# Performance work log

Measured on AMD Instinct MI355X. Metric: run time of the kernel, lower is better.

Reference implementation:

```python
import jax, jax.numpy as jnp
import numpy as np

N, D_IN, D_H, D_OUT, M = 256, 768, 768, 512, 100000


def setup_inputs() -> dict:
    key = jax.random.key(0)
    ks = jax.random.split(key, 8)
    img_feats = jax.random.normal(ks[0], (N, D_IN), dtype=jnp.float32)
    w1 = jax.random.normal(ks[1], (D_H, D_IN), dtype=jnp.float32) * (1.0 / np.sqrt(D_IN))
    b1 = jax.random.normal(ks[2], (D_H,), dtype=jnp.float32) * 0.01
    w2 = jax.random.normal(ks[3], (D_OUT, D_H), dtype=jnp.float32) * (1.0 / np.sqrt(D_H))
    b2 = jax.random.normal(ks[4], (D_OUT,), dtype=jnp.float32) * 0.01
    logit_scale = jnp.asarray(np.log(1.0 / 0.07), dtype=jnp.float32)
    loc = jax.random.normal(ks[5], (M, D_OUT), dtype=jnp.float32)
    loc_feats = loc / jnp.linalg.norm(loc, axis=1, keepdims=True)  # pre-normalized gallery
    gps_gallery = jax.random.uniform(ks[6], (M, 2), dtype=jnp.float32, minval=-90.0, maxval=90.0)
    return {
        "img_feats": img_feats, "w1": w1, "b1": b1, "w2": w2, "b2": b2,
        "logit_scale": logit_scale, "loc_feats": loc_feats,
        "gps_gallery": gps_gallery, "top_k": 5,
    }


def reference(img_feats, w1, b1, w2, b2, logit_scale, loc_feats, gps_gallery, top_k):
    # Tsfm MLP head: Linear -> ReLU -> Linear
    h = jax.nn.relu(img_feats @ w1.T + b1)            # [N, D_H]
    img = h @ w2.T + b2                               # [N, D_OUT]
    # F.normalize(dim=1)
    img_n = img / jnp.linalg.norm(img, axis=1, keepdims=True)
    # forward_cached: scaled cosine-similarity logits against 100K gallery
    logits = jnp.exp(logit_scale) * (img_n @ loc_feats.T)  # [N, M]
    # predict: softmax over full gallery row, then top-k retrieval
    probs = jax.nn.softmax(logits, axis=-1)
    top_vals, top_idx = jax.lax.top_k(probs, top_k)   # [N, k]
    top_pred_gps = gps_gallery[top_idx[0]]            # [k, 2] (first image, as in original)
    top_pred_prob = top_vals[0]                       # [k]
    return (logits, top_pred_gps, top_pred_prob)
```

## Files before the change

kernel.cpp:

```cpp
#include <hip/hip_runtime.h>
#include <math.h>

#define N_IMG 256
#define DIN   768
#define DH    768
#define DOUT  512
#define M_GAL 100000
#define CAP   2048
#define MT    1568

typedef __bf16 bf16_t;
typedef __bf16 bf16x8 __attribute__((ext_vector_type(8)));
typedef float  f32x4  __attribute__((ext_vector_type(4)));
typedef float  f32x16 __attribute__((ext_vector_type(16)));

#define OFF_H      0
#define OFF_IMG    (N_IMG*DH)
#define OFF_IMGN   (OFF_IMG  + N_IMG*DOUT)
#define OFF_IMGT   (OFF_IMGN + N_IMG*DOUT)
#define OFF_STATS  (OFF_IMGT + N_IMG*DOUT/2)
#define OFF_CIDX   (OFF_STATS + 4)
#define OFF_CVAL   (OFF_CIDX + CAP)

#define OUT_GPS  ((size_t)N_IMG * (size_t)M_GAL)
#define OUT_PROB (OUT_GPS + 10)

__device__ inline unsigned fkey(float x) {
  unsigned u = __float_as_uint(x);
  return (u & 0x80000000u) ? ~u : (u | 0x80000000u);
}
__device__ inline float fkey_inv(unsigned k) {
  unsigned u = (k & 0x80000000u) ? (k ^ 0x80000000u) : ~k;
  return __uint_as_float(u);
}

template<int KDIM, int NCOLS, bool RELU>
__global__ __launch_bounds__(256) void mlp_gemm(const float* __restrict__ A,
    const float* __restrict__ B, const float* __restrict__ bias,
    float* __restrict__ C, unsigned* stats_init) {
  if (stats_init && blockIdx.x == 0 && blockIdx.y == 0 && threadIdx.x == 0) {
    stats_init[0] = 0u; stats_init[1] = 0u; stats_init[2] = 0u;
  }
  __shared__ float As[32][34];
  __shared__ float Bs[32][34];
  const int t  = threadIdx.x;
  const int rowbase = blockIdx.y * 32;
  const int colbase = blockIdx.x * 32;
  const int sm = t >> 3;
  const int kc = (t & 7) << 2;
  const int ty = t >> 4, tx = t & 15;
  float a00 = 0.f, a01 = 0.f, a10 = 0.f, a11 = 0.f;
  for (int kt = 0; kt < KDIM; kt += 32) {
    float4 av = *(const float4*)(A + (size_t)(rowbase + sm) * KDIM + kt + kc);
    float4 bv = *(const float4*)(B + (size_t)(colbase + sm) * KDIM + kt + kc);
    __syncthreads();
    As[kc+0][sm] = av.x; As[kc+1][sm] = av.y; As[kc+2][sm] = av.z; As[kc+3][sm] = av.w;
    Bs[kc+0][sm] = bv.x; Bs[kc+1][sm] = bv.y; Bs[kc+2][sm] = bv.z; Bs[kc+3][sm] = bv.w;
    __syncthreads();
#pragma unroll
    for (int j = 0; j < 32; ++j) {
      float2 a = *(const float2*)(&As[j][2*ty]);
      float2 b = *(const float2*)(&Bs[j][2*tx]);
      a00 = fmaf(a.x, b.x, a00); a01 = fmaf(a.x, b.y, a01);
      a10 = fmaf(a.y, b.x, a10); a11 = fmaf(a.y, b.y, a11);
    }
  }
  const int r0 = rowbase + 2*ty;
  const int c0 = colbase + 2*tx;
  const float bb0 = bias[c0], bb1 = bias[c0+1];
  float v00 = a00 + bb0, v01 = a01 + bb1, v10 = a10 + bb0, v11 = a11 + bb1;
  if (RELU) {
    v00 = fmaxf(v00, 0.f); v01 = fmaxf(v01, 0.f);
    v10 = fmaxf(v10, 0.f); v11 = fmaxf(v11, 0.f);
  }
  C[(size_t)r0*NCOLS + c0]       = v00; C[(size_t)r0*NCOLS + c0 + 1]     = v01;
  C[(size_t)(r0+1)*NCOLS + c0]   = v10; C[(size_t)(r0+1)*NCOLS + c0 + 1] = v11;
}

__global__ __launch_bounds__(256) void norm_cast_kernel(const float* __restrict__ img,
    float* __restrict__ img_n, bf16_t* __restrict__ img_t) {
  const int row = blockIdx.x, t = threadIdx.x;
  const float v0 = img[row*DOUT + t];
  const float v1 = img[row*DOUT + 256 + t];
  float s = v0*v0 + v1*v1;
  for (int o = 32; o > 0; o >>= 1) s += __shfl_down(s, o);
  __shared__ float ws4[4];
  if ((t & 63) == 0) ws4[t >> 6] = s;
  __syncthreads();
  const float tot = ws4[0] + ws4[1] + ws4[2] + ws4[3];
  const float inv = 1.0f / sqrtf(tot);
  const float n0 = v0 * inv, n1 = v1 * inv;
  img_n[row*DOUT + t]       = n0;
  img_n[row*DOUT + 256 + t] = n1;
  const int k0 = t, k1 = t + 256;
  img_t[(((k0 >> 3)*N_IMG) + row)*8 + (k0 & 7)] = (bf16_t)n0;
  img_t[(((k1 >> 3)*N_IMG) + row)*8 + (k1 & 7)] = (bf16_t)n1;
}

__global__ __launch_bounds__(256, 5) void logits_kernel(const float* __restrict__ loc,
    const bf16_t* __restrict__ img_t, const float* __restrict__ ls,
    float* __restrict__ out, float* __restrict__ sumexp, unsigned* __restrict__ maxkey) {
  __shared__ bf16_t Bsl[2 * 8 * 64 * 8];
  const int t = threadIdx.x;
  const int w = t >> 6, l = t & 63;
  const int wi = w >> 1;
  const int wc = w & 1;
  const int hi = l >> 5;
  const int lo = l & 31;
  const int bx = blockIdx.x;
  const int mtile = (bx & 7) + (bx >> 4) * 8;
  const int h     = (bx >> 3) & 1;
  const int mb = mtile * 64;
  const int m  = mb + wc * 32 + lo;

  const int sk8 = t & 7, sr0 = t >> 3;
  const int gr0 = min(mb + sr0,      M_GAL - 1);
  const int gr1 = min(mb + 32 + sr0, M_GAL - 1);
  const float* sp0 = loc + (size_t)gr0 * 512 + sk8 * 8;
  const float* sp1 = loc + (size_t)gr1 * 512 + sk8 * 8;
  bf16_t* bw0 = Bsl + (sk8 * 64 + (sr0 ^ sk8)) * 8;
  bf16_t* bw1 = bw0 + 32 * 8;

  const bf16_t* ap = img_t + (size_t)(h * 128 + wi * 64 + lo) * 8;

  f32x16 acc[2];
  acc[0] = (f32x16)(0.f);
  acc[1] = (f32x16)(0.f);

  float4 r00, r01, r10, r11;

#define BLOAD(c_) {                                                   \
    const float* p0_ = sp0 + (c_) * 64;                               \
    const float* p1_ = sp1 + (c_) * 64;                               \
    r00 = *(const float4*)p0_; r01 = *(const float4*)(p0_ + 4);       \
    r10 = *(const float4*)p1_; r11 = *(const float4*)(p1_ + 4);       \
  }

#define BWRITE(pb_) {                                                 \
    bf16x8 b0_, b1_;                                                  \
    b0_[0] = (bf16_t)r00.x; b0_[1] = (bf16_t)r00.y;                   \
    b0_[2] = (bf16_t)r00.z; b0_[3] = (bf16_t)r00.w;                   \
    b0_[4] = (bf16_t)r01.x; b0_[5] = (bf16_t)r01.y;                   \
    b0_[6] = (bf16_t)r01.z; b0_[7] = (bf16_t)r01.w;                   \
    b1_[0] = (bf16_t)r10.x; b1_[1] = (bf16_t)r10.y;                   \
    b1_[2] = (bf16_t)r10.z; b1_[3] = (bf16_t)r10.w;                   \
    b1_[4] = (bf16_t)r11.x; b1_[5] = (bf16_t)r11.y;                   \
    b1_[6] = (bf16_t)r11.z; b1_[7] = (bf16_t)r11.w;                   \
    *(bf16x8*)(bw0 + (pb_) * 4096) = b0_;                             \
    *(bf16x8*)(bw1 + (pb_) * 4096) = b1_;                             \
  }

#define COMPUTE(kt, pb_) {                                            \
    const int kg_ = (kt) * 2 + hi;              \
    const int kl_ = ((kt) & 3) * 2 + hi;   \
    bf16x8 af_[2];                                                    \
    _Pragma("unroll")                                                 \
    for (int i_ = 0; i_ < 2; ++i_)                                    \
      af_[i_] = *(const bf16x8*)(ap + ((size_t)kg_ * 256 + i_ * 32) * 8); \
    const bf16x8 bf_ = *(const bf16x8*)(Bsl + ((pb_) * 4096 + (kl_ * 64 + ((wc * 32 + lo) ^ kl_)) * 8)); \
    _Pragma("unroll")                                                 \
    for (int i_ = 0; i_ < 2; ++i_)                                    \
      acc[i_] = __builtin_amdgcn_mfma_f32_32x32x16_bf16(af_[i_], bf_, acc[i_], 0, 0, 0); \
  }

  BLOAD(0);
  BWRITE(0);
  __syncthreads();

#pragma unroll
  for (int c = 0; c < 8; ++c) {
    const int pb = c & 1;
    if (c < 7) { BLOAD(c + 1); }
#pragma unroll
    for (int q = 0; q < 4; ++q) {
      COMPUTE(c * 4 + q, pb);
    }
    if (c < 7) {
      BWRITE(pb ^ 1);
      __syncthreads();
    }
  }
#undef BLOAD
#undef BWRITE
#undef COMPUTE

  const float scale = expf(ls[0]);
  if (h == 0 && wi == 0) {
    float mx = -1e30f, se = 0.f;
    if (hi == 0 && m < M_GAL) {
      const float v = scale * acc[0][0];
      mx = v;
      se = expf(v);
    }
#pragma unroll
    for (int o = 1; o < 64; o <<= 1) {
      mx = fmaxf(mx, __shfl_xor(mx, o));
      se += __shfl_xor(se, o);
    }
    if (l == 0) { atomicAdd(sumexp, se); atomicMax(maxkey, fkey(mx)); }
  }
  if (m < M_GAL) {
#pragma unroll
    for (int i = 0; i < 2; ++i) {
      const int ib = h * 128 + wi * 64 + i * 32 + hi * 4;
#pragma unroll
      for (int r = 0; r < 16; ++r) {
        const int img = ib + (r & 3) + 8 * (r >> 2);
        __builtin_nontemporal_store(scale * acc[i][r], out + (size_t)img * M_GAL + m);
      }
    }
  }
}

__global__ __launch_bounds__(256) void collect_kernel(const float* __restrict__ out,
    const unsigned* __restrict__ maxkey, unsigned* __restrict__ counter,
    int* __restrict__ cidx) {
  const int i = blockIdx.x * 256 + threadIdx.x;
  if (i >= M_GAL) return;
  const float thresh = fkey_inv(*maxkey) - 0.8f;
  if (out[i] > thresh) {
    const unsigned p = atomicAdd(counter, 1u);
    if (p < CAP) cidx[p] = i;
  }
}

__global__ __launch_bounds__(256) void recompute_kernel(const float* __restrict__ loc,
    const float* __restrict__ img_n, const float* __restrict__ ls,
    const unsigned* __restrict__ counter, const int* __restrict__ cidx,
    float* __restrict__ cval) {
  const int w = threadIdx.x >> 6, l = threadIdx.x & 63;
  const unsigned cnt = *counter;
  const int n = (int)(cnt < CAP ? cnt : CAP);
  const float scale = expf(ls[0]);
  for (int c = blockIdx.x * 4 + w; c < n; c += gridDim.x * 4) {
    const int idx = cidx[c];
    const float* B = loc + (size_t)idx * 512;
    float s = 0.f;
#pragma unroll
    for (int e = 0; e < 8; ++e) s = fmaf(img_n[l + e*64], B[l + e*64], s);
    for (int o = 32; o > 0; o >>= 1) s += __shfl_down(s, o);
    if (l == 0) cval[c] = scale * s;
  }
}

__global__ __launch_bounds__(256) void finalize_kernel(const unsigned* __restrict__ counter,
    const int* __restrict__ cidx, const float* __restrict__ cval,
    const float* __restrict__ gps, const float* __restrict__ sumexp,
    float* __restrict__ out) {
  __shared__ float v[CAP];
  __shared__ int   id[CAP];
  __shared__ float rv[256];
  __shared__ int   ri[256];
  __shared__ int   rs[256];
  const int t = threadIdx.x;
  const unsigned cnt = *counter;
  const int n = (int)(cnt < CAP ? cnt : CAP);
  for (int i = t; i < CAP; i += 256) {
    v[i]  = (i < n) ? cval[i] : -1e30f;
    id[i] = (i < n) ? cidx[i] : 0x7fffffff;
  }
  const float se = *sumexp;
  __syncthreads();
  for (int k = 0; k < 5; ++k) {
    float bv = -1e30f; int bidx = 0x7fffffff; int bslot = -1;
    for (int i = t; i < CAP; i += 256) {
      const float vi = v[i]; const int ii = id[i];
      if (vi > bv || (vi == bv && ii < bidx)) { bv = vi; bidx = ii; bslot = i; }
    }
    rv[t] = bv; ri[t] = bidx; rs[t] = bslot;
    __syncthreads();
    for (int s = 128; s > 0; s >>= 1) {
      if (t < s) {
        if (rv[t+s] > rv[t] || (rv[t+s] == rv[t] && ri[t+s] < ri[t])) {
          rv[t] = rv[t+s]; ri[t] = ri[t+s]; rs[t] = rs[t+s];
        }
      }
      __syncthreads();
    }
    if (t == 0) {
      const int sl = rs[0]; const int gi = ri[0]; const float lv = rv[0];
      float g0 = 0.f, g1 = 0.f, pr = 0.f;
      if (sl >= 0 && gi != 0x7fffffff) {
        g0 = gps[(size_t)gi*2]; g1 = gps[(size_t)gi*2 + 1];
        pr = expf(lv) / se;
        v[sl] = -1e30f; id[sl] = 0x7fffffff;
      }
      out[OUT_GPS + 2*k]     = g0;
      out[OUT_GPS + 2*k + 1] = g1;
      out[OUT_PROB + k]      = pr;
    }
    __syncthreads();
  }
}

extern "C" void kernel_launch(void* const* d_in, const int* in_sizes, int n_in,
                              void* d_out, int out_size, void* d_ws, size_t ws_size,
                              hipStream_t stream) {
  const float* img_feats = (const float*)d_in[0];
  const float* w1  = (const float*)d_in[1];
  const float* b1  = (const float*)d_in[2];
  const float* w2  = (const float*)d_in[3];
  const float* b2  = (const float*)d_in[4];
  const float* ls  = (const float*)d_in[5];
  const float* loc = (const float*)d_in[6];
  const float* gps = (const float*)d_in[7];
  float* out = (float*)d_out;
  float* ws  = (float*)d_ws;

  float*    h       = ws + OFF_H;
  float*    img     = ws + OFF_IMG;
  float*    img_n   = ws + OFF_IMGN;
  bf16_t*   img_t   = (bf16_t*)(ws + OFF_IMGT);
  float*    sumexp  = ws + OFF_STATS;
  unsigned* maxkey  = (unsigned*)(ws + OFF_STATS + 1);
  unsigned* counter = (unsigned*)(ws + OFF_STATS + 2);
  int*      cidx    = (int*)(ws + OFF_CIDX);
  float*    cval    = ws + OFF_CVAL;

  mlp_gemm<DIN, DH, true><<<dim3(DH/32, N_IMG/32), 256, 0, stream>>>(
      img_feats, w1, b1, h, (unsigned*)(ws + OFF_STATS));
  mlp_gemm<DH, DOUT, false><<<dim3(DOUT/32, N_IMG/32), 256, 0, stream>>>(
      h, w2, b2, img, nullptr);
  norm_cast_kernel<<<N_IMG, 256, 0, stream>>>(img, img_n, img_t);
  logits_kernel<<<MT * 2, 256, 0, stream>>>(loc, img_t, ls, out, sumexp, maxkey);
  collect_kernel<<<(M_GAL + 255) / 256, 256, 0, stream>>>(out, maxkey, counter, cidx);
  recompute_kernel<<<128, 256, 0, stream>>>(loc, img_n, ls, counter, cidx, cval);
  finalize_kernel<<<1, 256, 0, stream>>>(counter, cidx, cval, gps, sumexp, out);
}
```

Before: 455.7 us.

## Stage image operand tiles into LDS via async global_load_lds double buffering

The A operand (normalized image features in bf16) used to be read straight from global memory on every MFMA step. It is now copied into a double-buffered LDS tile with global_load_lds alongside the existing B staging, and the MFMA fragments are read from LDS. The goal is lower global/L2 traffic and load latency on the A side. In exchange the kernel uses an extra 32KB of shared memory and the occupancy hint drops from 5 to 3 blocks. There is also a risk that the async LDS loads are not fully ordered by the existing barrier without an explicit vmcnt wait.

```diff
diff --git a/kernel.cpp b/kernel.cpp
--- a/kernel.cpp
+++ b/kernel.cpp
@@ -97,9 +97,10 @@
   img_t[(((k1 >> 3)*N_IMG) + row)*8 + (k1 & 7)] = (bf16_t)n1;
 }
 
-__global__ __launch_bounds__(256, 5) void logits_kernel(const float* __restrict__ loc,
+__global__ __launch_bounds__(256, 3) void logits_kernel(const float* __restrict__ loc,
     const bf16_t* __restrict__ img_t, const float* __restrict__ ls,
     float* __restrict__ out, float* __restrict__ sumexp, unsigned* __restrict__ maxkey) {
+  __shared__ bf16_t Asl[2 * 8 * 128 * 8];
   __shared__ bf16_t Bsl[2 * 8 * 64 * 8];
   const int t = threadIdx.x;
   const int w = t >> 6, l = t & 63;
@@ -121,8 +122,6 @@
   bf16_t* bw0 = Bsl + (sk8 * 64 + (sr0 ^ sk8)) * 8;
   bf16_t* bw1 = bw0 + 32 * 8;
 
-  const bf16_t* ap = img_t + (size_t)(h * 128 + wi * 64 + lo) * 8;
-
   f32x16 acc[2];
   acc[0] = (f32x16)(0.f);
   acc[1] = (f32x16)(0.f);
@@ -150,38 +149,51 @@
     *(bf16x8*)(bw1 + (pb_) * 4096) = b1_;                             \
   }
 
-#define COMPUTE(kt, pb_) {                                            \
-    const int kg_ = (kt) * 2 + hi;              \
+#define STAGEA(c_, pa_) {                                             \
+    _Pragma("unroll")                                                 \
+    for (int r_ = 0; r_ < 4; ++r_) {                                  \
+      __builtin_amdgcn_global_load_lds(                               \
+          (__attribute__((address_space(1))) void*)(img_t + (((size_t)((c_) * 8 + r_ * 2 + (t >> 7)) * 256 + h * 128 + (t & 127))) * 8), \
+          (__attribute__((address_space(3))) void*)(Asl + (pa_) * 8192 + (r_ * 256 + t) * 8), \
+          16, 0, 0);                                                  \
+    } }
+
+#define COMPUTE(kt, pa_, pb_) {                                       \
     const int kl_ = ((kt) & 3) * 2 + hi;   \
     bf16x8 af_[2];                                                    \
     _Pragma("unroll")                                                 \
     for (int i_ = 0; i_ < 2; ++i_)                                    \
-      af_[i_] = *(const bf16x8*)(ap + ((size_t)kg_ * 256 + i_ * 32) * 8); \
-    const bf16x8 bf_ = *(const bf16x8*)(Bsl + ((pb_) * 4096 + (kl_ * 64 + ((wc * 32 + lo) ^ kl_)) * 8)); \
+      af_[i_] = *(const bf16x8*)(Asl + (pa_) * 8192 + (kl_ * 128 + wi * 64 + i_ * 32 + lo) * 8); \
+    const bf16x8 bf_ = *(const bf16x8*)(Bsl + (pb_) * 4096 + (kl_ * 64 + ((wc * 32 + lo) ^ kl_)) * 8); \
     _Pragma("unroll")                                                 \
     for (int i_ = 0; i_ < 2; ++i_)                                    \
       acc[i_] = __builtin_amdgcn_mfma_f32_32x32x16_bf16(af_[i_], bf_, acc[i_], 0, 0, 0); \
   }
 
   BLOAD(0);
+  STAGEA(0, 0);
   BWRITE(0);
   __syncthreads();
 
 #pragma unroll
   for (int c = 0; c < 8; ++c) {
-    const int pb = c & 1;
-    if (c < 7) { BLOAD(c + 1); }
+    const int pp = c & 1;
+    if (c < 7) {
+      BLOAD(c + 1);
+      STAGEA(c + 1, pp ^ 1);
+    }
 #pragma unroll
     for (int q = 0; q < 4; ++q) {
-      COMPUTE(c * 4 + q, pb);
+      COMPUTE(c * 4 + q, pp, pp);
     }
     if (c < 7) {
-      BWRITE(pb ^ 1);
+      BWRITE(pp ^ 1);
       __syncthreads();
     }
   }
 #undef BLOAD
 #undef BWRITE
+#undef STAGEA
 #undef COMPUTE
 
   const float scale = expf(ls[0]);
```

After: 437.6 us. 1.04x faster.
